# Performance work log

Hardware: AMD Instinct MI355X
Metric: run time of the kernel (lower is better)

The kernel has to match this reference:

```python
import jax, jax.numpy as jnp
import numpy as np

N = 200000      # total points
B = 4           # number of point clouds
C_IN = 128
C_OUT = 256
GRID = 0.05
EPS = 1e-5      # BatchNorm eps


def setup_inputs() -> dict:
    key = jax.random.key(0)
    ks = jax.random.split(key, 9)
    xyz = jax.random.uniform(ks[0], (1, N, 3), dtype=jnp.float32)
    features = jax.random.normal(ks[1], (1, N, C_IN), dtype=jnp.float32)
    offset = jnp.array([50000, 100000, 150000, 200000], dtype=jnp.int32)
    W1 = jax.random.normal(ks[2], (C_OUT, C_IN), dtype=jnp.float32) * 0.02
    b1 = jax.random.normal(ks[3], (C_OUT,), dtype=jnp.float32) * 0.01
    gamma = jax.random.uniform(ks[4], (C_OUT,), dtype=jnp.float32, minval=0.5, maxval=1.5)
    beta = jax.random.normal(ks[5], (C_OUT,), dtype=jnp.float32) * 0.1
    W2 = jax.random.normal(ks[6], (C_OUT, C_OUT), dtype=jnp.float32) * 0.02
    b2 = jax.random.normal(ks[7], (C_OUT,), dtype=jnp.float32) * 0.01
    return {"xyz": xyz, "features": features, "offset": offset,
            "W1": W1, "b1": b1, "gamma": gamma, "beta": beta, "W2": W2, "b2": b2}


def _offset2batch(offset, n):
    counts = jnp.diff(jnp.concatenate([jnp.zeros((1,), offset.dtype), offset]))
    return jnp.repeat(jnp.arange(offset.shape[0], dtype=jnp.int32), counts,
                      total_repeat_length=n)


def reference(xyz, features, offset, W1, b1, gamma, beta, W2, b2):
    pos = xyz[0]          # [N, 3]
    x = features[0]       # [N, C_IN]
    batch = _offset2batch(offset, pos.shape[0])  # [N]

    # fc: 1x1 conv == linear; BatchNorm1d in training mode (batch stats, biased var)
    h = x @ W1.T + b1                                   # [N, C_OUT]
    mu = h.mean(axis=0)
    var = h.var(axis=0)
    h = (h - mu) / jnp.sqrt(var + EPS) * gamma + beta
    h = jax.nn.relu(h)
    feats = h @ W2.T + b2                               # [N, C_OUT]

    # per-batch min corner (start)
    start = jax.ops.segment_min(pos, batch, num_segments=B)   # [B, 3]

    # voxel grid clustering
    coords = jnp.floor((pos - start[batch]) / GRID).astype(jnp.int32)  # [N, 3] >= 0
    dims = coords.max(axis=0) + 1
    lin = ((batch * dims[0] + coords[:, 0]) * dims[1] + coords[:, 1]) * dims[2] + coords[:, 2]

    uniq, inv, counts = jnp.unique(lin, return_inverse=True, return_counts=True)
    M = uniq.shape[0]

    # segment_csr mean / max over voxels (order-independent, equals sorted CSR reduce)
    xyz_out = jax.ops.segment_sum(pos, inv, num_segments=M) / counts[:, None].astype(pos.dtype)
    feat_out = jax.ops.segment_max(feats, inv, num_segments=M)

    seg_batch = jax.ops.segment_max(batch, inv, num_segments=M)
    offset_out = jnp.cumsum(jnp.bincount(seg_batch, length=B)).astype(offset.dtype)

    return (xyz_out[None], feat_out[None], offset_out, inv)
```

## Files before the change

kernel.cpp:

```cpp
#include <hip/hip_runtime.h>
#include <stdint.h>

#define GRID_SZ 0.05f
#define BN_EPS 1e-5f

typedef __attribute__((ext_vector_type(8))) short bf16x8;
typedef __attribute__((ext_vector_type(4))) float f32x4;

#define WS_START   0
#define WS_DIMS    64
#define WS_CHSUM   128
#define WS_CHSQ    1152
#define WS_AC      2176
#define WS_BC      3200
#define WS_W1B     4224
#define WS_W2B     69760
#define WS_GRAM    200832
#define WS_CSUM    266368
#define WS_HIST    266880
#define WS_RANK    529024
#define WS_CURS    791296
#define WS_BSUM    1053440
#define WS_XYZS    1053952
#define WS_LIN     1840384
#define WS_PERM    2640384
#define WS_XB      3440384

__device__ __forceinline__ short f2bf(float f) {
  unsigned u = __float_as_uint(f);
  u += 0x7FFFu + ((u >> 16) & 1u);
  return (short)(u >> 16);
}

__device__ __forceinline__ bf16x8 load_frag(const float* p) {
  f32x4 a = *(const f32x4*)p;
  f32x4 b = *(const f32x4*)(p + 4);
  bf16x8 r;
  r[0] = f2bf(a[0]); r[1] = f2bf(a[1]); r[2] = f2bf(a[2]); r[3] = f2bf(a[3]);
  r[4] = f2bf(b[0]); r[5] = f2bf(b[1]); r[6] = f2bf(b[2]); r[7] = f2bf(b[3]);
  return r;
}

__device__ __forceinline__ int batch_of(int p, const int* offs, int nb) {
  int b = 0;
  while (b < nb - 1 && p >= offs[b]) b++;
  return b;
}

__global__ void k_conv(const float* __restrict__ src, short* __restrict__ dst, size_t n8) {
  size_t i = (size_t)blockIdx.x * blockDim.x + threadIdx.x;
  size_t stride = (size_t)gridDim.x * blockDim.x;
  for (; i < n8; i += stride)
    *(bf16x8*)(dst + i * 8) = load_frag(src + i * 8);
}

__global__ void k_convw(const float* __restrict__ W1, const float* __restrict__ W2,
                        short* __restrict__ W1b, short* __restrict__ W2b) {
  int i = blockIdx.x * blockDim.x + threadIdx.x;
  if (i < 4096) *(bf16x8*)(W1b + i * 8) = load_frag(W1 + i * 8);
  else { int j = i - 4096; *(bf16x8*)(W2b + j * 8) = load_frag(W2 + j * 8); }
}

__global__ void k_init(unsigned* featU, size_t featN, int* hist, float* xyzs,
                       float* chsum, float* chsq, float* gram, float* csum,
                       unsigned* gstart, int* gdims) {
  size_t i = (size_t)blockIdx.x * blockDim.x + threadIdx.x;
  size_t stride = (size_t)gridDim.x * blockDim.x;
  for (size_t j = i; j < featN; j += stride) featU[j] = 0u;
  for (size_t j = i; j < 65536; j += stride) hist[j] = 0;
  for (size_t j = i; j < 65536u * 3; j += stride) xyzs[j] = 0.f;
  for (size_t j = i; j < 16384; j += stride) gram[j] = 0.f;
  if (i < 256) { chsum[i] = 0.f; chsq[i] = 0.f; }
  if (i < 128) csum[i] = 0.f;
  if (i < 12) gstart[i] = 0x7F800000u;
  if (i < 3) gdims[i] = 0;
}

__global__ void k_min(const float* __restrict__ pos, const int* __restrict__ offs,
                      int N, int nb, unsigned* gstart) {
  __shared__ unsigned smin[12];
  int tid = threadIdx.x;
  if (tid < 12) smin[tid] = 0x7F800000u;
  __syncthreads();
  int p = blockIdx.x * blockDim.x + tid;
  if (p < N) {
    int b = batch_of(p, offs, nb);
    for (int c = 0; c < 3; c++)
      atomicMin(&smin[b * 3 + c], __float_as_uint(pos[p * 3 + c]));
  }
  __syncthreads();
  if (tid < 3 * nb) atomicMin(&gstart[tid], smin[tid]);
}

__global__ void k_dims(const float* __restrict__ pos, const int* __restrict__ offs,
                       int N, int nb, const unsigned* gstart, int* gdims) {
  __shared__ int sd[3];
  int tid = threadIdx.x;
  if (tid < 3) sd[tid] = 0;
  __syncthreads();
  int p = blockIdx.x * blockDim.x + tid;
  if (p < N) {
    int b = batch_of(p, offs, nb);
    for (int c = 0; c < 3; c++) {
      float s = __uint_as_float(gstart[b * 3 + c]);
      int cc = (int)floorf((pos[p * 3 + c] - s) / GRID_SZ);
      atomicMax(&sd[c], cc);
    }
  }
  __syncthreads();
  if (tid < 3) atomicMax(&gdims[tid], sd[tid]);
}

__global__ void k_hist(const float* __restrict__ pos, const int* __restrict__ offs,
                       int N, int nb, const unsigned* gstart, const int* gdims,
                       int* lin, int* hist, float* xyzs) {
  int p = blockIdx.x * blockDim.x + threadIdx.x;
  if (p >= N) return;
  int b = batch_of(p, offs, nb);
  int d0 = gdims[0] + 1, d1 = gdims[1] + 1, d2 = gdims[2] + 1;
  int c[3];
  for (int i = 0; i < 3; i++) {
    float s = __uint_as_float(gstart[b * 3 + i]);
    c[i] = (int)floorf((pos[p * 3 + i] - s) / GRID_SZ);
  }
  int li = ((b * d0 + c[0]) * d1 + c[1]) * d2 + c[2];
  if (li < 0 || li >= 65536) li = 0;
  lin[p] = li;
  atomicAdd(&hist[li], 1);
  atomicAdd(&xyzs[li * 3 + 0], pos[p * 3 + 0]);
  atomicAdd(&xyzs[li * 3 + 1], pos[p * 3 + 1]);
  atomicAdd(&xyzs[li * 3 + 2], pos[p * 3 + 2]);
}

__global__ __launch_bounds__(1024) void k_scanA(const int* __restrict__ hist,
                                                const int* __restrict__ gdims, int nb,
                                                int2* bsum) {
  __shared__ int so[16], sc2[16];
  int d0 = gdims[0] + 1, d1 = gdims[1] + 1, d2 = gdims[2] + 1;
  int bins = nb * d0 * d1 * d2;
  if (bins > 65536) bins = 65536;
  int i = blockIdx.x * 1024 + threadIdx.x;
  int o = 0, c = 0;
  if (i < bins) { int h = hist[i]; o = (h > 0); c = h; }
  for (int d = 1; d < 64; d <<= 1) { o += __shfl_xor(o, d); c += __shfl_xor(c, d); }
  int w = threadIdx.x >> 6;
  if ((threadIdx.x & 63) == 0) { so[w] = o; sc2[w] = c; }
  __syncthreads();
  if (threadIdx.x == 0) {
    int O = 0, C = 0;
    for (int k = 0; k < 16; k++) { O += so[k]; C += sc2[k]; }
    bsum[blockIdx.x] = make_int2(O, C);
  }
}

__global__ __launch_bounds__(1024) void k_scanB(const int* __restrict__ hist,
                                                const int* __restrict__ gdims, int nb,
                                                const int2* __restrict__ bsum,
                                                int* rank, int* cursor) {
  __shared__ int so[1024], sc2[1024];
  __shared__ int sbase[2];
  int d0 = gdims[0] + 1, d1 = gdims[1] + 1, d2 = gdims[2] + 1;
  int bins = nb * d0 * d1 * d2;
  if (bins > 65536) bins = 65536;
  int b = blockIdx.x;
  int tid = threadIdx.x;
  if (tid == 0) {
    int O = 0, C = 0;
    for (int k = 0; k < b; k++) { int2 s = bsum[k]; O += s.x; C += s.y; }
    sbase[0] = O; sbase[1] = C;
  }
  int i = b * 1024 + tid;
  int h = (i < bins) ? hist[i] : 0;
  int o = (h > 0), c = h;
  so[tid] = o; sc2[tid] = c;
  __syncthreads();
  for (int off = 1; off < 1024; off <<= 1) {
    int vo = (tid >= off) ? so[tid - off] : 0;
    int vc = (tid >= off) ? sc2[tid - off] : 0;
    __syncthreads();
    so[tid] += vo; sc2[tid] += vc;
    __syncthreads();
  }
  if (i < bins) {
    rank[i]   = sbase[0] + so[tid] - o;
    cursor[i] = sbase[1] + sc2[tid] - c;
  }
  if (i == bins - 1) rank[bins] = sbase[0] + so[tid];
}

__global__ void k_scatter(const int* __restrict__ lin, const int* __restrict__ rank,
                          int* cursor, int N, int* __restrict__ perm,
                          float* __restrict__ out_inv) {
  int p = blockIdx.x * blockDim.x + threadIdx.x;
  if (p >= N) return;
  int li = lin[p];
  out_inv[p] = (float)rank[li];
  int slot = atomicAdd(&cursor[li], 1);
  perm[slot] = p;
}

__global__ void k_voxfin(const int* __restrict__ hist, const int* __restrict__ rank,
                         const float* __restrict__ xyzs, const int* __restrict__ gdims,
                         int nb, float* out_xyz, float* out_off) {
  int d0 = gdims[0] + 1, d1 = gdims[1] + 1, d2 = gdims[2] + 1;
  int dxyz = d0 * d1 * d2;
  int bins = nb * dxyz;
  if (bins > 65536) bins = 65536;
  int i = blockIdx.x * blockDim.x + threadIdx.x;
  if (blockIdx.x == 0 && (int)threadIdx.x < nb) {
    int t = (int)threadIdx.x;
    int idx = (t + 1) * dxyz; if (idx > bins) idx = bins;
    out_off[t] = (float)rank[idx];
  }
  if (i >= bins) return;
  int cnt = hist[i];
  if (cnt <= 0) return;
  int v = rank[i];
  float fc = (float)cnt;
  out_xyz[v * 3 + 0] = xyzs[i * 3 + 0] / fc;
  out_xyz[v * 3 + 1] = xyzs[i * 3 + 1] / fc;
  out_xyz[v * 3 + 2] = xyzs[i * 3 + 2] / fc;
}

#define GCHUNK 1024
__global__ __launch_bounds__(256, 2) void k_gram(const short* __restrict__ Xb, int N,
                                                 float* __restrict__ gram,
                                                 float* __restrict__ csum) {
  __shared__ short xt[128 * 72];
  __shared__ float lcs[128];
  int tid = threadIdx.x;
  int wid = tid >> 6, lane = tid & 63;
  int lr = lane & 15, lg = lane >> 4;
  int base = blockIdx.x * GCHUNK;
  int cg = tid & 7;
  float cs[16];
#pragma unroll
  for (int j = 0; j < 16; j++) cs[j] = 0.f;
  f32x4 acc[2][8];
#pragma unroll
  for (int a = 0; a < 2; a++)
#pragma unroll
    for (int b = 0; b < 8; b++) acc[a][b] = (f32x4){0.f, 0.f, 0.f, 0.f};

  for (int k0 = 0; k0 < GCHUNK; k0 += 64) {
    __syncthreads();
#pragma unroll
    for (int it = 0; it < 2; it++) {
      int task = tid + it * 256;
      int r = task >> 3;
      int row = base + k0 + r;
      bf16x8 v0 = {0,0,0,0,0,0,0,0}, v1 = {0,0,0,0,0,0,0,0};
      if (row < N) {
        const short* src = Xb + (size_t)row * 128 + cg * 16;
        v0 = *(const bf16x8*)src;
        v1 = *(const bf16x8*)(src + 8);
      }
#pragma unroll
      for (int j = 0; j < 8; j++) {
        cs[j]     += __uint_as_float(((unsigned)(unsigned short)v0[j]) << 16);
        cs[j + 8] += __uint_as_float(((unsigned)(unsigned short)v1[j]) << 16);
      }
      int rs = r ^ (cg << 3);
#pragma unroll
      for (int j = 0; j < 8; j++) {
        xt[(cg * 16 + j) * 72 + rs]     = v0[j];
        xt[(cg * 16 + 8 + j) * 72 + rs] = v1[j];
      }
    }
    __syncthreads();
#pragma unroll
    for (int ks = 0; ks < 2; ks++) {
      int kk = ks * 32 + lg * 8;
      bf16x8 f[8], af[2];
#pragma unroll
      for (int s = 0; s < 8; s++)
        f[s] = *(const bf16x8*)(xt + (s * 16 + lr) * 72 + (kk ^ (s << 3)));
#pragma unroll
      for (int a = 0; a < 2; a++) {
        int ti = wid * 2 + a;
        af[a] = *(const bf16x8*)(xt + (ti * 16 + lr) * 72 + (kk ^ (ti << 3)));
      }
#pragma unroll
      for (int a = 0; a < 2; a++)
#pragma unroll
        for (int b = 0; b < 8; b++)
          acc[a][b] = __builtin_amdgcn_mfma_f32_16x16x32_bf16(af[a], f[b], acc[a][b], 0, 0, 0);
    }
  }
#pragma unroll
  for (int a = 0; a < 2; a++)
#pragma unroll
    for (int b = 0; b < 8; b++)
#pragma unroll
      for (int r_ = 0; r_ < 4; r_++) {
        int ci = (wid * 2 + a) * 16 + lg * 4 + r_;
        int cj = b * 16 + lr;
        atomicAdd(&gram[ci * 128 + cj], acc[a][b][r_]);
      }
  if (tid < 128) lcs[tid] = 0.f;
  __syncthreads();
#pragma unroll
  for (int j = 0; j < 16; j++) atomicAdd(&lcs[cg * 16 + j], cs[j]);
  __syncthreads();
  if (tid < 128) atomicAdd(&csum[tid], lcs[tid]);
}

__global__ __launch_bounds__(128) void k_finalizeG(const float* __restrict__ gram,
                                                   const float* __restrict__ csum,
                                                   const float* __restrict__ W1,
                                                   const float* __restrict__ b1,
                                                   const float* __restrict__ gamma,
                                                   const float* __restrict__ beta,
                                                   int N, float* Ac, float* Bc) {
  __shared__ float w[128], red[128], red2[128];
  int c = blockIdx.x, j = threadIdx.x;
  w[j] = W1[c * 128 + j];
  __syncthreads();
  float t = 0.f;
  for (int k = 0; k < 128; k++) t += gram[k * 128 + j] * w[k];
  red[j]  = t * w[j];
  red2[j] = w[j] * csum[j];
  __syncthreads();
  for (int off = 64; off > 0; off >>= 1) {
    if (j < off) { red[j] += red[j + off]; red2[j] += red2[j + off]; }
    __syncthreads();
  }
  if (j == 0) {
    float fn = (float)N;
    float q  = red[0] / fn;
    float md = red2[0] / fn;
    float b  = b1[c];
    float mu = md + b;
    float e2 = q + 2.f * b * md + b * b;
    float var = e2 - mu * mu;
    float s = gamma[c] * rsqrtf(var + BN_EPS);
    Ac[c] = s;
    Bc[c] = (b - mu) * s + beta[c];
  }
}

__global__ __launch_bounds__(256) void k_statsA(const float* __restrict__ X,
                                                const short* __restrict__ W1b,
                                                const float* __restrict__ b1, int N,
                                                float* chsum, float* chsq) {
  int tid = threadIdx.x;
  int wid = tid >> 6, lane = tid & 63;
  int lr = lane & 15, lg = lane >> 4;
  int p0 = blockIdx.x * 64;
  int wcol = wid * 64;
  f32x4 acc[4][4] = {};
  for (int kk = 0; kk < 4; kk++) {
    int k = kk * 32 + lg * 8;
    bf16x8 af[4], bfr[4];
    for (int m = 0; m < 4; m++) {
      int row = p0 + m * 16 + lr; if (row >= N) row = N - 1;
      af[m] = load_frag(X + (size_t)row * 128 + k);
    }
    for (int n = 0; n < 4; n++)
      bfr[n] = *(const bf16x8*)(W1b + (size_t)(wcol + n * 16 + lr) * 128 + k);
    for (int m = 0; m < 4; m++)
      for (int n = 0; n < 4; n++)
        acc[m][n] = __builtin_amdgcn_mfma_f32_16x16x32_bf16(af[m], bfr[n], acc[m][n], 0, 0, 0);
  }
  for (int n = 0; n < 4; n++) {
    int c = wcol + n * 16 + lr;
    float bv = b1[c];
    float s1 = 0.f, s2 = 0.f;
    for (int m = 0; m < 4; m++)
      for (int r = 0; r < 4; r++) {
        int row = p0 + m * 16 + lg * 4 + r;
        if (row < N) {
          float h = acc[m][n][r] + bv;
          s1 += h; s2 += h * h;
        }
      }
    s1 += __shfl_xor(s1, 16); s2 += __shfl_xor(s2, 16);
    s1 += __shfl_xor(s1, 32); s2 += __shfl_xor(s2, 32);
    if (lg == 0) { atomicAdd(&chsum[c], s1); atomicAdd(&chsq[c], s2); }
  }
}

__global__ void k_finalize(const float* chsum, const float* chsq, const float* b1,
                           const float* gamma, const float* beta, int N,
                           float* Ac, float* Bc) {
  int c = threadIdx.x;
  float fn = (float)N;
  float mu = chsum[c] / fn;
  float var = chsq[c] / fn - mu * mu;
  float s = gamma[c] * rsqrtf(var + BN_EPS);
  Ac[c] = s;
  Bc[c] = (b1[c] - mu) * s + beta[c];
}

template <bool XBF>
__global__ __launch_bounds__(256, 3) void k_gemmB(const float* __restrict__ X,
                                                  const short* __restrict__ Xb,
                                                  const short* __restrict__ W1b,
                                                  const short* __restrict__ W2b,
                                                  const float* __restrict__ b2,
                                                  const float* __restrict__ Ac,
                                                  const float* __restrict__ Bc,
                                                  const int* __restrict__ perm,
                                                  const int* __restrict__ lin,
                                                  const int* __restrict__ rank,
                                                  int N, unsigned* __restrict__ featU) {
  __shared__ char smem[64 * 264 * 2];
  __shared__ int vox_s[64];
  __shared__ int perm_s[64];
  char* ylds = smem;
  unsigned short* lmax = (unsigned short*)smem;

  int tid = threadIdx.x;
  int wid = tid >> 6, lane = tid & 63;
  int lr = lane & 15, lg = lane >> 4;
  int p0 = blockIdx.x * 64;
  int wcol = wid * 64;

  if (tid < 64) {
    int s = p0 + tid;
    int pp = perm[(s < N) ? s : (N - 1)];
    perm_s[tid] = pp;
    vox_s[tid] = (s < N) ? rank[lin[pp]] : -1;
  }
  __syncthreads();

  f32x4 acc[4][4] = {};
  for (int kk = 0; kk < 4; kk++) {
    int k = kk * 32 + lg * 8;
    bf16x8 af[4], bfr[4];
    for (int m = 0; m < 4; m++) {
      int row = perm_s[m * 16 + lr];
      if (XBF) af[m] = *(const bf16x8*)(Xb + (size_t)row * 128 + k);
      else     af[m] = load_frag(X + (size_t)row * 128 + k);
    }
    for (int n = 0; n < 4; n++)
      bfr[n] = *(const bf16x8*)(W1b + (size_t)(wcol + n * 16 + lr) * 128 + k);
    for (int m = 0; m < 4; m++)
      for (int n = 0; n < 4; n++)
        acc[m][n] = __builtin_amdgcn_mfma_f32_16x16x32_bf16(af[m], bfr[n], acc[m][n], 0, 0, 0);
  }

  for (int n = 0; n < 4; n++) {
    int c = wcol + n * 16 + lr;
    float Av = Ac[c], Bv = Bc[c];
    int colb = c * 2;
    for (int m = 0; m < 4; m++)
      for (int r = 0; r < 4; r++) {
        int row = m * 16 + lg * 4 + r;
        float y = fmaxf(acc[m][n][r] * Av + Bv, 0.0f);
        int addr = (row * 512 + colb) ^ ((row & 7) << 4);
        *(short*)(ylds + addr) = f2bf(y);
      }
  }
  __syncthreads();

  f32x4 acc2[4][4] = {};
  for (int kk = 0; kk < 8; kk++) {
    int k = kk * 32 + lg * 8;
    int kb = k * 2;
    bf16x8 af[4], bfr[4];
    for (int m = 0; m < 4; m++) {
      int row = m * 16 + lr;
      af[m] = *(const bf16x8*)(ylds + ((row * 512 + kb) ^ ((row & 7) << 4)));
    }
    for (int n = 0; n < 4; n++)
      bfr[n] = *(const bf16x8*)(W2b + (size_t)(wcol + n * 16 + lr) * 256 + k);
    for (int m = 0; m < 4; m++)
      for (int n = 0; n < 4; n++)
        acc2[m][n] = __builtin_amdgcn_mfma_f32_16x16x32_bf16(af[m], bfr[n], acc2[m][n], 0, 0, 0);
  }
  __syncthreads();

  for (int n = 0; n < 4; n++) {
    int c = wcol + n * 16 + lr;
    float bv = b2[c];
    for (int m = 0; m < 4; m++)
      for (int r = 0; r < 4; r++) {
        int row = m * 16 + lg * 4 + r;
        unsigned us = (unsigned)(unsigned short)f2bf(acc2[m][n][r] + bv);
        us = (us & 0x8000u) ? (~us & 0xFFFFu) : (us | 0x8000u);
        lmax[row * 264 + c] = (unsigned short)us;
      }
  }
  __syncthreads();

  int nrows = N - p0; if (nrows > 64) nrows = 64;
  int c = tid;
  unsigned run = 0;
  int vprev = vox_s[0];
  int run_start = 0;
  for (int row = 0; row < nrows; row++) {
    int v = vox_s[row];
    if (v != vprev) {
      size_t idx = (size_t)vprev * 256 + c;
      if (run_start > 0) featU[idx] = run << 16;
      else atomicMax(&featU[idx], run << 16);
      run = 0; vprev = v; run_start = row;
    }
    run = max(run, (unsigned)lmax[row * 264 + c]);
  }
  atomicMax(&featU[(size_t)vprev * 256 + c], run << 16);
}

__global__ void k_decode(unsigned* featU, size_t n) {
  size_t i = (size_t)blockIdx.x * blockDim.x + threadIdx.x;
  size_t stride = (size_t)gridDim.x * blockDim.x;
  for (; i < n; i += stride) {
    unsigned e = featU[i] >> 16;
    unsigned us = (e & 0x8000u) ? (e & 0x7FFFu) : (~e & 0xFFFFu);
    ((float*)featU)[i] = __uint_as_float(us << 16);
  }
}

extern "C" void kernel_launch(void* const* d_in, const int* in_sizes, int n_in,
                              void* d_out, int out_size, void* d_ws, size_t ws_size,
                              hipStream_t stream) {
  const float* xyz   = (const float*)d_in[0];
  const float* X     = (const float*)d_in[1];
  const int*   offs  = (const int*)d_in[2];
  const float* W1    = (const float*)d_in[3];
  const float* b1    = (const float*)d_in[4];
  const float* gamma = (const float*)d_in[5];
  const float* beta  = (const float*)d_in[6];
  const float* W2    = (const float*)d_in[7];
  const float* b2    = (const float*)d_in[8];

  int N  = in_sizes[0] / 3;
  int nb = in_sizes[2];
  int M  = (out_size - nb - N) / 259;
  if (M <= 0) return;

  char* ws = (char*)d_ws;
  unsigned* gstart = (unsigned*)(ws + WS_START);
  int*   gdims  = (int*)(ws + WS_DIMS);
  float* chsum  = (float*)(ws + WS_CHSUM);
  float* chsq   = (float*)(ws + WS_CHSQ);
  float* Ac     = (float*)(ws + WS_AC);
  float* Bc     = (float*)(ws + WS_BC);
  short* W1b    = (short*)(ws + WS_W1B);
  short* W2b    = (short*)(ws + WS_W2B);
  float* gram   = (float*)(ws + WS_GRAM);
  float* csum   = (float*)(ws + WS_CSUM);
  int*   hist   = (int*)(ws + WS_HIST);
  int*   rank   = (int*)(ws + WS_RANK);
  int*   cursor = (int*)(ws + WS_CURS);
  int2*  bsum   = (int2*)(ws + WS_BSUM);
  float* xyzs   = (float*)(ws + WS_XYZS);
  int*   lin    = (int*)(ws + WS_LIN);
  int*   perm   = (int*)(ws + WS_PERM);
  short* Xb     = (short*)(ws + WS_XB);

  size_t req = (size_t)WS_XB + (size_t)N * 128 * 2;
  bool xbf = ws_size >= req;

  float* out_xyz  = (float*)d_out;
  float* out_feat = out_xyz + (size_t)3 * M;
  float* out_off  = out_feat + (size_t)M * 256;
  float* out_inv  = out_off + nb;
  unsigned* featU = (unsigned*)out_feat;

  int npb = (N + 255) / 256;
  int ngb = (N + 63) / 64;
  int ngr = (N + GCHUNK - 1) / GCHUNK;

  hipLaunchKernelGGL(k_init, dim3(2048), dim3(256), 0, stream,
                     featU, (size_t)M * 256, hist, xyzs, chsum, chsq, gram, csum,
                     gstart, gdims);
  hipLaunchKernelGGL(k_convw, dim3(24), dim3(256), 0, stream, W1, W2, W1b, W2b);
  if (xbf) {
    hipLaunchKernelGGL(k_conv, dim3(4096), dim3(256), 0, stream, X, Xb, (size_t)N * 128 / 8);
    hipLaunchKernelGGL(k_gram, dim3(ngr), dim3(256), 0, stream, Xb, N, gram, csum);
  }
  hipLaunchKernelGGL(k_min, dim3(npb), dim3(256), 0, stream, xyz, offs, N, nb, gstart);
  hipLaunchKernelGGL(k_dims, dim3(npb), dim3(256), 0, stream, xyz, offs, N, nb, gstart, gdims);
  hipLaunchKernelGGL(k_hist, dim3(npb), dim3(256), 0, stream,
                     xyz, offs, N, nb, gstart, gdims, lin, hist, xyzs);
  hipLaunchKernelGGL(k_scanA, dim3(64), dim3(1024), 0, stream, hist, gdims, nb, bsum);
  hipLaunchKernelGGL(k_scanB, dim3(64), dim3(1024), 0, stream,
                     hist, gdims, nb, bsum, rank, cursor);
  hipLaunchKernelGGL(k_voxfin, dim3(256), dim3(256), 0, stream,
                     hist, rank, xyzs, gdims, nb, out_xyz, out_off);
  hipLaunchKernelGGL(k_scatter, dim3(npb), dim3(256), 0, stream,
                     lin, rank, cursor, N, perm, out_inv);
  if (xbf) {
    hipLaunchKernelGGL(k_finalizeG, dim3(256), dim3(128), 0, stream,
                       gram, csum, W1, b1, gamma, beta, N, Ac, Bc);
    hipLaunchKernelGGL((k_gemmB<true>), dim3(ngb), dim3(256), 0, stream,
                       X, Xb, W1b, W2b, b2, Ac, Bc, perm, lin, rank, N, featU);
  } else {
    hipLaunchKernelGGL(k_statsA, dim3(ngb), dim3(256), 0, stream,
                       X, W1b, b1, N, chsum, chsq);
    hipLaunchKernelGGL(k_finalize, dim3(1), dim3(256), 0, stream,
                       chsum, chsq, b1, gamma, beta, N, Ac, Bc);
    hipLaunchKernelGGL((k_gemmB<false>), dim3(ngb), dim3(256), 0, stream,
                       X, Xb, W1b, W2b, b2, Ac, Bc, perm, lin, rank, N, featU);
  }
  hipLaunchKernelGGL(k_decode, dim3(2048), dim3(256), 0, stream,
                     featU, (size_t)M * 256);
}
```

Measured before the change: 312.5 us.

## Write interior voxel maxima as decoded floats and decode only boundary voxels

The voxel max epilogue now stores the LDS staging tile column-major with an XOR swizzle, so each thread loads its channel strip with eight vector reads instead of 64 strided scalar reads. Voxels that lie entirely inside one block are written straight as decoded floats. Only voxels that touch a block boundary go through atomicMax, and these are marked in a per-voxel flag array that reuses the scan cursor buffer. The decode pass then reads the flag and rewrites only the marked voxels, which cuts its read-modify-write traffic. In exchange it relies on the cursor buffer being free at this point and on the magic value never colliding with leftover cursor contents.

After: 314.4 us. About the same (+0.6%).

```diff
diff --git a/kernel.cpp b/kernel.cpp
--- a/kernel.cpp
+++ b/kernel.cpp
@@ -3,8 +3,10 @@
 
 #define GRID_SZ 0.05f
 #define BN_EPS 1e-5f
+#define FLAG_MAGIC 0x7FECA110
 
 typedef __attribute__((ext_vector_type(8))) short bf16x8;
+typedef __attribute__((ext_vector_type(8))) unsigned short u16x8;
 typedef __attribute__((ext_vector_type(4))) float f32x4;
 
 #define WS_START   0
@@ -47,6 +49,11 @@
   return b;
 }
 
+__device__ __forceinline__ float dec16(unsigned e) {
+  unsigned us = (e & 0x8000u) ? (e & 0x7FFFu) : (~e & 0xFFFFu);
+  return __uint_as_float(us << 16);
+}
+
 __global__ void k_conv(const float* __restrict__ src, short* __restrict__ dst, size_t n8) {
   size_t i = (size_t)blockIdx.x * blockDim.x + threadIdx.x;
   size_t stride = (size_t)gridDim.x * blockDim.x;
@@ -403,8 +410,9 @@
                                                   const int* __restrict__ perm,
                                                   const int* __restrict__ lin,
                                                   const int* __restrict__ rank,
-                                                  int N, unsigned* __restrict__ featU) {
-  __shared__ char smem[64 * 264 * 2];
+                                                  int N, unsigned* __restrict__ featU,
+                                                  int* __restrict__ bflag) {
+  __shared__ char smem[64 * 256 * 2];
   __shared__ int vox_s[64];
   __shared__ int perm_s[64];
   char* ylds = smem;
@@ -474,41 +482,63 @@
   for (int n = 0; n < 4; n++) {
     int c = wcol + n * 16 + lr;
     float bv = b2[c];
+    int cbase = c << 6;
+    int cswz = (c & 7) << 3;
     for (int m = 0; m < 4; m++)
       for (int r = 0; r < 4; r++) {
         int row = m * 16 + lg * 4 + r;
         unsigned us = (unsigned)(unsigned short)f2bf(acc2[m][n][r] + bv);
         us = (us & 0x8000u) ? (~us & 0xFFFFu) : (us | 0x8000u);
-        lmax[row * 264 + c] = (unsigned short)us;
-      }
-  }
-  __syncthreads();
+        lmax[cbase | (row ^ cswz)] = (unsigned short)us;
+      }
+  }
+  __syncthreads();
+
+  int c = tid;
+  int s_ = c & 7;
+  const unsigned short* strip = lmax + (c << 6);
+  u16x8 ch[8];
+#pragma unroll
+  for (int j = 0; j < 8; j++)
+    ch[j] = *(const u16x8*)(strip + ((j ^ s_) << 3));
 
   int nrows = N - p0; if (nrows > 64) nrows = 64;
-  int c = tid;
   unsigned run = 0;
   int vprev = vox_s[0];
   int run_start = 0;
-  for (int row = 0; row < nrows; row++) {
-    int v = vox_s[row];
-    if (v != vprev) {
-      size_t idx = (size_t)vprev * 256 + c;
-      if (run_start > 0) featU[idx] = run << 16;
-      else atomicMax(&featU[idx], run << 16);
-      run = 0; vprev = v; run_start = row;
-    }
-    run = max(run, (unsigned)lmax[row * 264 + c]);
+#pragma unroll
+  for (int j = 0; j < 8; j++) {
+#pragma unroll
+    for (int t = 0; t < 8; t++) {
+      int row = j * 8 + t;
+      if (row < nrows) {
+        int v = vox_s[row];
+        if (v != vprev) {
+          size_t idx = (size_t)vprev * 256 + c;
+          if (run_start > 0) {
+            ((float*)featU)[idx] = dec16(run);
+          } else {
+            atomicMax(&featU[idx], run << 16);
+            if (tid == 0) bflag[vprev] = FLAG_MAGIC;
+          }
+          run = 0; vprev = v; run_start = row;
+        }
+        run = max(run, (unsigned)ch[j][t]);
+      }
+    }
   }
   atomicMax(&featU[(size_t)vprev * 256 + c], run << 16);
-}
-
-__global__ void k_decode(unsigned* featU, size_t n) {
+  if (tid == 0) bflag[vprev] = FLAG_MAGIC;
+}
+
+__global__ void k_decode(unsigned* featU, const int* __restrict__ bflag, size_t n) {
   size_t i = (size_t)blockIdx.x * blockDim.x + threadIdx.x;
   size_t stride = (size_t)gridDim.x * blockDim.x;
   for (; i < n; i += stride) {
-    unsigned e = featU[i] >> 16;
-    unsigned us = (e & 0x8000u) ? (e & 0x7FFFu) : (~e & 0xFFFFu);
-    ((float*)featU)[i] = __uint_as_float(us << 16);
+    if (bflag[i >> 8] == FLAG_MAGIC) {
+      unsigned e = featU[i] >> 16;
+      ((float*)featU)[i] = dec16(e);
+    }
   }
 }
 
@@ -586,15 +616,15 @@
     hipLaunchKernelGGL(k_finalizeG, dim3(256), dim3(128), 0, stream,
                        gram, csum, W1, b1, gamma, beta, N, Ac, Bc);
     hipLaunchKernelGGL((k_gemmB<true>), dim3(ngb), dim3(256), 0, stream,
-                       X, Xb, W1b, W2b, b2, Ac, Bc, perm, lin, rank, N, featU);
+                       X, Xb, W1b, W2b, b2, Ac, Bc, perm, lin, rank, N, featU, cursor);
   } else {
     hipLaunchKernelGGL(k_statsA, dim3(ngb), dim3(256), 0, stream,
                        X, W1b, b1, N, chsum, chsq);
     hipLaunchKernelGGL(k_finalize, dim3(1), dim3(256), 0, stream,
                        chsum, chsq, b1, gamma, beta, N, Ac, Bc);
     hipLaunchKernelGGL((k_gemmB<false>), dim3(ngb), dim3(256), 0, stream,
-                       X, Xb, W1b, W2b, b2, Ac, Bc, perm, lin, rank, N, featU);
+                       X, Xb, W1b, W2b, b2, Ac, Bc, perm, lin, rank, N, featU, cursor);
   }
   hipLaunchKernelGGL(k_decode, dim3(2048), dim3(256), 0, stream,
-                     featU, (size_t)M * 256);
-}
+                     featU, cursor, (size_t)M * 256);
+}
```
